# Kernel optimization log

Measured on AMD Instinct MI355X. Metric: run time of the kernel, lower is better.

The kernel has to match this reference:

```python
import jax, jax.numpy as jnp
import numpy as np

B, T, E, H = 4, 2048, 1024, 1024

def setup_inputs() -> dict:
    key = jax.random.key(0)
    k1, k2, k3, k4 = jax.random.split(key, 4)
    inputs = jax.random.normal(k1, (B, T, E), dtype=jnp.float32)
    # Dense(size, use_bias=False) -> weight [emb, size], glorot-ish scale
    Wq = jax.random.normal(k2, (E, H), dtype=jnp.float32) * (1.0 / np.sqrt(E))
    Wk = jax.random.normal(k3, (E, H), dtype=jnp.float32) * (1.0 / np.sqrt(E))
    Wv = jax.random.normal(k4, (E, H), dtype=jnp.float32) * (1.0 / np.sqrt(E))
    return {"inputs": inputs, "Wq": Wq, "Wk": Wk, "Wv": Wv}

def reference(inputs, Wq, Wk, Wv):
    # inputs: [B, T, E]
    _, Tc, Ec = inputs.shape
    q = inputs @ Wq  # [B, T, H]
    k = inputs @ Wk  # [B, T, H]
    v = inputs @ Wv  # [B, T, H]
    # scores scaled by emb_dim**-0.5 (NOT head size) as in the source
    w = jnp.einsum('bih,bjh->bij', q, k) * (Ec ** -0.5)  # [B, T, T]
    tril = jnp.tril(jnp.ones((Tc, Tc), dtype=bool))
    w = jnp.where(tril, w, -jnp.inf)
    # NOTE: source uses softmax over axis=1 (query axis), non-standard but faithful
    w = jax.nn.softmax(w, axis=1)
    # dropout_rate=0.0 -> identity
    out = w @ v  # [B, T, H]
    return out
```

## Files before the change

### kernel.cpp

```cpp
#include <hip/hip_runtime.h>
#include <hip/hip_bf16.h>
#include <stdint.h>


typedef short bf16x8 __attribute__((ext_vector_type(8)));
typedef float f32x4  __attribute__((ext_vector_type(4)));

__device__ __forceinline__ unsigned short f2bf(float f) {
    union { float f; unsigned u; } x; x.f = f;
    unsigned r = x.u + 0x7FFFu + ((x.u >> 16) & 1u);
    return (unsigned short)(r >> 16);
}
__device__ __forceinline__ float bf2f(unsigned short h) {
    union { unsigned u; float f; } x; x.u = ((unsigned)h) << 16;
    return x.f;
}

__global__ __launch_bounds__(256) void prep_kernel(
    const float* __restrict__ X,
    const float* __restrict__ Wq, const float* __restrict__ Wk,
    const float* __restrict__ Wv,
    unsigned short* __restrict__ Xb, unsigned short* __restrict__ WT)
{
    __shared__ unsigned short tile[64][65];
    unsigned id = blockIdx.x;
    if (id < 8192) {
        size_t i = ((size_t)id * 256 + threadIdx.x) * 4;
        float4 v = *(const float4*)(X + i);
        union { unsigned short h[4]; unsigned long long u; } p;
        p.h[0] = f2bf(v.x); p.h[1] = f2bf(v.y);
        p.h[2] = f2bf(v.z); p.h[3] = f2bf(v.w);
        *(unsigned long long*)(Xb + i) = p.u;
    } else {
        unsigned w = id - 8192;
        unsigned which = w >> 8;
        const float* W = (which == 0) ? Wq : (which == 1) ? Wk : Wv;
        unsigned short* out = WT + (size_t)which * 1024 * 1024;
        const int R = 1024, C = 1024;
        unsigned t2 = w & 255;
        int c0 = (int)(t2 & 15) * 64, r0 = (int)(t2 >> 4) * 64;
        int tx = threadIdx.x & 63, ty = threadIdx.x >> 6;
#pragma unroll
        for (int i = 0; i < 16; ++i) {
            int r = ty + i * 4;
            tile[r][tx] = f2bf(W[(size_t)(r0 + r) * C + c0 + tx]);
        }
        __syncthreads();
#pragma unroll
        for (int i = 0; i < 16; ++i) {
            int c = ty + i * 4;
            out[(size_t)(c0 + c) * R + r0 + tx] = tile[tx][c];
        }
    }
}

__global__ __launch_bounds__(256, 3) void gemm_nt_qkv(
    const unsigned short* __restrict__ A, const unsigned short* __restrict__ B,
    unsigned short* __restrict__ Cout, unsigned short* __restrict__ C2,
    unsigned short* __restrict__ C3, int K, int ldt)
{
    unsigned id = blockIdx.y * gridDim.x + blockIdx.x;
    unsigned xcd = id & 7, k2 = id >> 3;
    int tm = (int)(xcd * 8 + (k2 & 7));
    int tn = (int)(k2 >> 3);
    int m0 = tm * 128, n0 = tn * 128;
    int kmax = K;

    __shared__ unsigned short sAB[2 * 128 * 64];
    char* sAc = (char*)sAB;
    char* sBc = (char*)sAB + 16384;

    unsigned t = threadIdx.x, lane = t & 63, wave = t >> 6;

    unsigned srow = t >> 2;
    unsigned gsw = (t & 3) ^ ((t >> 3) & 3);
    const unsigned short* pA = A + (size_t)(m0 + srow) * K + gsw * 8;
    const unsigned short* pB = B + (size_t)(n0 + srow) * K + gsw * 8;
    const size_t rstep = (size_t)64 * K;
    unsigned ldsOff = t * 16;

    unsigned wm = (wave >> 1) * 64, wn = (wave & 1) * 64;
    unsigned lrow = lane & 15;
    unsigned lk = ((lane >> 4) ^ ((lane >> 1) & 3)) * 8;
    const short* sAs = (const short*)sAB;
    const short* sBs = (const short*)(sAB + 128 * 64);

    f32x4 acc[4][4] = {};

    int4 rA0 = *(const int4*)(pA);
    int4 rA1 = *(const int4*)(pA + rstep);
    int4 rA2 = *(const int4*)(pA + 32);
    int4 rA3 = *(const int4*)(pA + rstep + 32);
    int4 rB0 = *(const int4*)(pB);
    int4 rB1 = *(const int4*)(pB + rstep);
    int4 rB2 = *(const int4*)(pB + 32);
    int4 rB3 = *(const int4*)(pB + rstep + 32);

    for (int k0 = 0; k0 < kmax; k0 += 64) {
        __syncthreads();
        *(int4*)(sAc + ldsOff)         = rA0;
        *(int4*)(sAc + ldsOff + 4096)  = rA1;
        *(int4*)(sAc + ldsOff + 8192)  = rA2;
        *(int4*)(sAc + ldsOff + 12288) = rA3;
        *(int4*)(sBc + ldsOff)         = rB0;
        *(int4*)(sBc + ldsOff + 4096)  = rB1;
        *(int4*)(sBc + ldsOff + 8192)  = rB2;
        *(int4*)(sBc + ldsOff + 12288) = rB3;
        __syncthreads();

        if (k0 + 64 < kmax) {
            pA += 64; pB += 64;
            rA0 = *(const int4*)(pA);
            rA1 = *(const int4*)(pA + rstep);
            rA2 = *(const int4*)(pA + 32);
            rA3 = *(const int4*)(pA + rstep + 32);
            rB0 = *(const int4*)(pB);
            rB1 = *(const int4*)(pB + rstep);
            rB2 = *(const int4*)(pB + 32);
            rB3 = *(const int4*)(pB + rstep + 32);
        }

#pragma unroll
        for (int kk = 0; kk < 2; ++kk) {
            bf16x8 a[4], b[4];
#pragma unroll
            for (int i = 0; i < 4; ++i) {
                a[i] = *(const bf16x8*)(sAs + kk * 4096 + (wm + i * 16 + lrow) * 32 + lk);
                b[i] = *(const bf16x8*)(sBs + kk * 4096 + (wn + i * 16 + lrow) * 32 + lk);
            }
#pragma unroll
            for (int i = 0; i < 4; ++i)
#pragma unroll
                for (int j = 0; j < 4; ++j)
                    acc[i][j] = __builtin_amdgcn_mfma_f32_16x16x32_bf16(
                        a[i], b[j], acc[i][j], 0, 0, 0);
        }
    }

    unsigned col = lane & 15, rq = (lane >> 4) * 4;
    if (n0 < 2048) {
        unsigned short* C = (n0 < 1024) ? Cout : C2;
        int nb = n0 & 1023;
#pragma unroll
        for (int i = 0; i < 4; ++i)
#pragma unroll
            for (int j = 0; j < 4; ++j)
#pragma unroll
                for (int r = 0; r < 4; ++r)
                    C[(size_t)(m0 + wm + i * 16 + rq + r) * 1024 + nb + wn + j * 16 + col] =
                        f2bf(acc[i][j][r]);
    } else {
        int batch = m0 >> 11, tb = m0 & 2047;
        unsigned short* C = C3 + (size_t)batch * 1024 * 2048;
#pragma unroll
        for (int i = 0; i < 4; ++i)
#pragma unroll
            for (int j = 0; j < 4; ++j) {
                union { unsigned short h[4]; unsigned long long u; } p;
#pragma unroll
                for (int r = 0; r < 4; ++r) p.h[r] = f2bf(acc[i][j][r]);
                int h = (n0 - 2048) + wn + j * 16 + col;
                int t0 = tb + wm + i * 16 + rq;
                *(unsigned long long*)(C + (size_t)h * ldt + t0) = p.u;
            }
    }
}

__global__ __launch_bounds__(256, 4) void scores64_kernel(
    const unsigned short* __restrict__ A, const unsigned short* __restrict__ B,
    unsigned short* __restrict__ Eb, float* __restrict__ fpar, float scale)
{
    int bz = blockIdx.z;
    unsigned bx = blockIdx.x;
    int u = (int)((bx & 7u) * 34u + (bx >> 3));
    int tm = (int)((sqrtf(4.f * (float)u + 1.f) - 1.f) * 0.5f);
    while ((tm + 1) * (tm + 2) <= u) ++tm;
    while (tm * (tm + 1) > u) --tm;
    int tn64 = u - tm * (tm + 1);
    const int K = 1024;
    int m0 = tm * 128, n0 = tn64 * 64;
    A += (size_t)bz * (size_t)2048 * 1024;
    B += (size_t)bz * (size_t)2048 * 1024;

    __shared__ unsigned short sAB[12288];
    char* sAc = (char*)sAB;
    char* sBc = (char*)sAB + 16384;

    unsigned t = threadIdx.x, lane = t & 63, wave = t >> 6;
    unsigned srow = t >> 2;
    unsigned gsw = (t & 3) ^ ((t >> 3) & 3);
    const unsigned short* pA = A + (size_t)(m0 + srow) * K + gsw * 8;
    const unsigned short* pB = B + (size_t)(n0 + srow) * K + gsw * 8;
    const size_t rstep = (size_t)64 * K;
    unsigned ldsOff = t * 16;

    unsigned wm = (wave >> 1) * 64, wn = (wave & 1) * 32;
    unsigned lrow = lane & 15;
    unsigned lk = ((lane >> 4) ^ ((lane >> 1) & 3)) * 8;
    const short* sAs = (const short*)sAB;
    const short* sBs = (const short*)(sAB + 8192);

    f32x4 acc[4][2] = {};

    int4 rA0 = *(const int4*)(pA);
    int4 rA1 = *(const int4*)(pA + rstep);
    int4 rA2 = *(const int4*)(pA + 32);
    int4 rA3 = *(const int4*)(pA + rstep + 32);
    int4 rB0 = *(const int4*)(pB);
    int4 rB1 = *(const int4*)(pB + 32);

    for (int k0 = 0; k0 < K; k0 += 64) {
        __syncthreads();
        *(int4*)(sAc + ldsOff)         = rA0;
        *(int4*)(sAc + ldsOff + 4096)  = rA1;
        *(int4*)(sAc + ldsOff + 8192)  = rA2;
        *(int4*)(sAc + ldsOff + 12288) = rA3;
        *(int4*)(sBc + ldsOff)         = rB0;
        *(int4*)(sBc + ldsOff + 4096)  = rB1;
        __syncthreads();

        if (k0 + 64 < K) {
            pA += 64; pB += 64;
            rA0 = *(const int4*)(pA);
            rA1 = *(const int4*)(pA + rstep);
            rA2 = *(const int4*)(pA + 32);
            rA3 = *(const int4*)(pA + rstep + 32);
            rB0 = *(const int4*)(pB);
            rB1 = *(const int4*)(pB + 32);
        }

#pragma unroll
        for (int kk = 0; kk < 2; ++kk) {
            bf16x8 a[4], b[2];
#pragma unroll
            for (int i = 0; i < 4; ++i)
                a[i] = *(const bf16x8*)(sAs + kk * 4096 + (wm + i * 16 + lrow) * 32 + lk);
#pragma unroll
            for (int j = 0; j < 2; ++j)
                b[j] = *(const bf16x8*)(sBs + kk * 2048 + (wn + j * 16 + lrow) * 32 + lk);
#pragma unroll
            for (int i = 0; i < 4; ++i)
#pragma unroll
                for (int j = 0; j < 2; ++j)
                    acc[i][j] = __builtin_amdgcn_mfma_f32_16x16x32_bf16(
                        a[i], b[j], acc[i][j], 0, 0, 0);
        }
    }

    unsigned col = lane & 15, rq = (lane >> 4) * 4;
    unsigned short* Ebp = Eb + (size_t)bz * (size_t)2048 * 2048;
    float* par = fpar + (size_t)bz * 32 * 2048;
    bool diag = ((tn64 >> 1) == tm);
    unsigned short* tile = sAB;
    __syncthreads();
#pragma unroll
    for (int jj = 0; jj < 2; ++jj) {
        float csum = 0.f;
        int jl = (int)(wn + jj * 16 + col);
        int jg = n0 + jl;
#pragma unroll
        for (int ii = 0; ii < 4; ++ii) {
#pragma unroll
            for (int r = 0; r < 4; ++r) {
                int il = (int)(wm + ii * 16 + rq + r);
                int ig = m0 + il;
                unsigned short us = 0;
                if (!diag || ig >= jg)
                    us = f2bf(__expf(acc[ii][jj][r] * scale));
                tile[il * 64 + jl] = us;
                csum += bf2f(us);
            }
        }
        csum += __shfl_xor(csum, 16);
        csum += __shfl_xor(csum, 32);
        if (lane < 16) {
            int rh = (m0 + (int)wm) >> 6;
            par[(size_t)rh * 2048 + n0 + wn + jj * 16 + lane] = csum;
        }
    }
    __syncthreads();
    {
        unsigned rr = t >> 3, cc = (t & 7) * 8;
#pragma unroll
        for (int p = 0; p < 4; ++p) {
            int li = (int)(p * 32 + rr);
            int4 v = *(const int4*)(tile + li * 64 + cc);
            *(int4*)(Ebp + (size_t)(m0 + li) * 2048 + n0 + cc) = v;
        }
    }
}

__global__ __launch_bounds__(256, 4) void pv64_kernel(
    const unsigned short* __restrict__ A, const unsigned short* __restrict__ B,
    float* __restrict__ out)
{
    unsigned id = blockIdx.x;
    int tm = 15 - (int)(id >> 6);
    unsigned rest = id & 63u;
    int bz = (int)(rest >> 4);
    int tn64 = (int)(rest & 15u);
    const int K = 2048;
    int m0 = tm * 128, n0 = tn64 * 64;
    int kmax = m0 + 128;
    A += (size_t)bz * (size_t)2048 * 2048;
    B += (size_t)bz * (size_t)1024 * 2048;

    __shared__ unsigned short sAB[12288];
    char* sAc = (char*)sAB;
    char* sBc = (char*)sAB + 16384;

    unsigned t = threadIdx.x, lane = t & 63, wave = t >> 6;
    unsigned srow = t >> 2;
    unsigned gsw = (t & 3) ^ ((t >> 3) & 3);
    const unsigned short* pA = A + (size_t)(m0 + srow) * K + gsw * 8;
    const unsigned short* pB = B + (size_t)(n0 + srow) * K + gsw * 8;
    const size_t rstep = (size_t)64 * K;
    unsigned ldsOff = t * 16;

    unsigned wm = (wave >> 1) * 64, wn = (wave & 1) * 32;
    unsigned lrow = lane & 15;
    unsigned lk = ((lane >> 4) ^ ((lane >> 1) & 3)) * 8;
    const short* sAs = (const short*)sAB;
    const short* sBs = (const short*)(sAB + 8192);

    f32x4 acc[4][2] = {};

    int4 rA0 = *(const int4*)(pA);
    int4 rA1 = *(const int4*)(pA + rstep);
    int4 rA2 = *(const int4*)(pA + 32);
    int4 rA3 = *(const int4*)(pA + rstep + 32);
    int4 rB0 = *(const int4*)(pB);
    int4 rB1 = *(const int4*)(pB + 32);

    for (int k0 = 0; k0 < kmax; k0 += 64) {
        __syncthreads();
        *(int4*)(sAc + ldsOff)         = rA0;
        *(int4*)(sAc + ldsOff + 4096)  = rA1;
        *(int4*)(sAc + ldsOff + 8192)  = rA2;
        *(int4*)(sAc + ldsOff + 12288) = rA3;
        *(int4*)(sBc + ldsOff)         = rB0;
        *(int4*)(sBc + ldsOff + 4096)  = rB1;
        __syncthreads();

        if (k0 + 64 < kmax) {
            pA += 64; pB += 64;
            rA0 = *(const int4*)(pA);
            rA1 = *(const int4*)(pA + rstep);
            rA2 = *(const int4*)(pA + 32);
            rA3 = *(const int4*)(pA + rstep + 32);
            rB0 = *(const int4*)(pB);
            rB1 = *(const int4*)(pB + 32);
        }

#pragma unroll
        for (int kk = 0; kk < 2; ++kk) {
            bf16x8 a[4], b[2];
#pragma unroll
            for (int i = 0; i < 4; ++i)
                a[i] = *(const bf16x8*)(sAs + kk * 4096 + (wm + i * 16 + lrow) * 32 + lk);
#pragma unroll
            for (int j = 0; j < 2; ++j)
                b[j] = *(const bf16x8*)(sBs + kk * 2048 + (wn + j * 16 + lrow) * 32 + lk);
#pragma unroll
            for (int i = 0; i < 4; ++i)
#pragma unroll
                for (int j = 0; j < 2; ++j)
                    acc[i][j] = __builtin_amdgcn_mfma_f32_16x16x32_bf16(
                        a[i], b[j], acc[i][j], 0, 0, 0);
        }
    }

    unsigned col = lane & 15, rq = (lane >> 4) * 4;
    float* C = out + (size_t)bz * (size_t)2048 * 1024;
#pragma unroll
    for (int i = 0; i < 4; ++i)
#pragma unroll
        for (int j = 0; j < 2; ++j)
#pragma unroll
            for (int r = 0; r < 4; ++r)
                C[(size_t)(m0 + wm + i * 16 + rq + r) * 1024 + n0 + wn + j * 16 + col] =
                    acc[i][j][r];
}

__global__ __launch_bounds__(256) void colsum_scale(
    const float* __restrict__ par, unsigned short* __restrict__ Vt)
{
    int b = blockIdx.z, t0 = blockIdx.x * 64, h0 = blockIdx.y * 128;
    __shared__ float Ls[64];
    int tid = threadIdx.x;
    if (tid < 64) {
        int j = t0 + tid;
        const float* p = par + (size_t)b * 32 * 2048;
        float s = 0.f;
        for (int rh = j >> 6; rh < 32; ++rh) s += p[(size_t)rh * 2048 + j];
        Ls[tid] = 1.0f / s;
    }
    __syncthreads();
    unsigned short* V = Vt + ((size_t)b << 21);
    int c8 = (tid & 7) * 8;
#pragma unroll
    for (int rr = 0; rr < 4; ++rr) {
        int h = h0 + rr * 32 + (tid >> 3);
        size_t idx = (size_t)h * 2048 + t0 + c8;
        bf16x8 v = *(bf16x8*)(V + idx);
#pragma unroll
        for (int e = 0; e < 8; ++e)
            v[e] = (short)f2bf(bf2f((unsigned short)v[e]) * Ls[c8 + e]);
        *(bf16x8*)(V + idx) = v;
    }
}

extern "C" void kernel_launch(void* const* d_in, const int* in_sizes, int n_in,
                              void* d_out, int out_size, void* d_ws, size_t ws_size,
                              hipStream_t stream)
{
    const int B = 4, T = 2048, E = 1024, H = 1024;
    const int M = B * T;
    const float* X  = (const float*)d_in[0];
    const float* Wq = (const float*)d_in[1];
    const float* Wk = (const float*)d_in[2];
    const float* Wv = (const float*)d_in[3];
    float* out = (float*)d_out;
    char* ws = (char*)d_ws;
    const size_t MB = 1024 * 1024;

    unsigned short* Xb  = (unsigned short*)(ws + 0);
    unsigned short* WqT = (unsigned short*)(ws + 16 * MB);
    unsigned short* Qb  = (unsigned short*)(ws + 32 * MB);
    unsigned short* Kb  = (unsigned short*)(ws + 48 * MB);
    unsigned short* Vt  = (unsigned short*)(ws + 64 * MB);
    unsigned short* Eb  = (unsigned short*)(ws + 0);
    float*          par  = (float*)d_out;

    prep_kernel<<<dim3(8960), 256, 0, stream>>>(X, Wq, Wk, Wv, Xb, WqT);

    gemm_nt_qkv<<<dim3(24, 64, 1), 256, 0, stream>>>(
        Xb, WqT, Qb, Kb, Vt, E, T);

    scores64_kernel<<<dim3(272, 1, B), 256, 0, stream>>>(
        Qb, Kb, Eb, par, 0.03125f);

    colsum_scale<<<dim3(32, 8, 4), 256, 0, stream>>>(par, Vt);

    pv64_kernel<<<dim3(1024), 256, 0, stream>>>(Eb, Vt, out);
}
```

Measured before the change: 233.6 us.

## Widen PV GEMM tile to 128x128 and split QKV GEMM into two launches

The causal P·V kernel now uses 128x128 output tiles with a 4x4 MFMA accumulator per wave, replacing the 128x64 tiles. This halves the block count and doubles reuse of each loaded A tile. The blocks are ordered so that long and short causal rows from different batches pair up. Separately, the QKV projection GEMM is split into two launches over halves of the M tiles. This costs an extra launch and lowers occupancy in the PV kernel, since each thread holds more registers.

```diff
diff --git a/kernel.cpp b/kernel.cpp
--- a/kernel.cpp
+++ b/kernel.cpp
@@ -57,12 +57,12 @@
 __global__ __launch_bounds__(256, 3) void gemm_nt_qkv(
     const unsigned short* __restrict__ A, const unsigned short* __restrict__ B,
     unsigned short* __restrict__ Cout, unsigned short* __restrict__ C2,
-    unsigned short* __restrict__ C3, int K, int ldt)
+    unsigned short* __restrict__ C3, int K, int ldt, int tmoff)
 {
     unsigned id = blockIdx.y * gridDim.x + blockIdx.x;
     unsigned xcd = id & 7, k2 = id >> 3;
-    int tm = (int)(xcd * 8 + (k2 & 7));
-    int tn = (int)(k2 >> 3);
+    int tm = (int)(xcd * 4 + (k2 & 3)) + tmoff;
+    int tn = (int)(k2 >> 2);
     int m0 = tm * 128, n0 = tn * 128;
     int kmax = K;
 
@@ -290,26 +290,27 @@
     }
 }
 
-__global__ __launch_bounds__(256, 4) void pv64_kernel(
+__global__ __launch_bounds__(256, 3) void pv128_kernel(
     const unsigned short* __restrict__ A, const unsigned short* __restrict__ B,
     float* __restrict__ out)
 {
-    unsigned id = blockIdx.x;
-    int tm = 15 - (int)(id >> 6);
-    unsigned rest = id & 63u;
-    int bz = (int)(rest >> 4);
-    int tn64 = (int)(rest & 15u);
-    const int K = 2048;
-    int m0 = tm * 128, n0 = tn64 * 64;
+    unsigned n = blockIdx.x;
+    int tn = (int)(n & 7u);
+    unsigned q = n >> 3, half = q >> 5, r = q & 31u;
+    int bz = (int)((half ? 2u : 0u) + (r & 1u));
+    int tm = half ? (int)(r >> 1) : (int)(15u - (r >> 1));
+    const int K = 2048, N = 1024;
+    int m0 = tm * 128, n0 = tn * 128;
     int kmax = m0 + 128;
     A += (size_t)bz * (size_t)2048 * 2048;
     B += (size_t)bz * (size_t)1024 * 2048;
 
-    __shared__ unsigned short sAB[12288];
+    __shared__ unsigned short sAB[2 * 128 * 64];
     char* sAc = (char*)sAB;
     char* sBc = (char*)sAB + 16384;
 
     unsigned t = threadIdx.x, lane = t & 63, wave = t >> 6;
+
     unsigned srow = t >> 2;
     unsigned gsw = (t & 3) ^ ((t >> 3) & 3);
     const unsigned short* pA = A + (size_t)(m0 + srow) * K + gsw * 8;
@@ -317,20 +318,22 @@
     const size_t rstep = (size_t)64 * K;
     unsigned ldsOff = t * 16;
 
-    unsigned wm = (wave >> 1) * 64, wn = (wave & 1) * 32;
+    unsigned wm = (wave >> 1) * 64, wn = (wave & 1) * 64;
     unsigned lrow = lane & 15;
     unsigned lk = ((lane >> 4) ^ ((lane >> 1) & 3)) * 8;
     const short* sAs = (const short*)sAB;
-    const short* sBs = (const short*)(sAB + 8192);
-
-    f32x4 acc[4][2] = {};
+    const short* sBs = (const short*)(sAB + 128 * 64);
+
+    f32x4 acc[4][4] = {};
 
     int4 rA0 = *(const int4*)(pA);
     int4 rA1 = *(const int4*)(pA + rstep);
     int4 rA2 = *(const int4*)(pA + 32);
     int4 rA3 = *(const int4*)(pA + rstep + 32);
     int4 rB0 = *(const int4*)(pB);
-    int4 rB1 = *(const int4*)(pB + 32);
+    int4 rB1 = *(const int4*)(pB + rstep);
+    int4 rB2 = *(const int4*)(pB + 32);
+    int4 rB3 = *(const int4*)(pB + rstep + 32);
 
     for (int k0 = 0; k0 < kmax; k0 += 64) {
         __syncthreads();
@@ -340,6 +343,8 @@
         *(int4*)(sAc + ldsOff + 12288) = rA3;
         *(int4*)(sBc + ldsOff)         = rB0;
         *(int4*)(sBc + ldsOff + 4096)  = rB1;
+        *(int4*)(sBc + ldsOff + 8192)  = rB2;
+        *(int4*)(sBc + ldsOff + 12288) = rB3;
         __syncthreads();
 
         if (k0 + 64 < kmax) {
@@ -349,22 +354,23 @@
             rA2 = *(const int4*)(pA + 32);
             rA3 = *(const int4*)(pA + rstep + 32);
             rB0 = *(const int4*)(pB);
-            rB1 = *(const int4*)(pB + 32);
+            rB1 = *(const int4*)(pB + rstep);
+            rB2 = *(const int4*)(pB + 32);
+            rB3 = *(const int4*)(pB + rstep + 32);
         }
 
 #pragma unroll
         for (int kk = 0; kk < 2; ++kk) {
-            bf16x8 a[4], b[2];
+            bf16x8 a[4], b[4];
+#pragma unroll
+            for (int i = 0; i < 4; ++i) {
+                a[i] = *(const bf16x8*)(sAs + kk * 4096 + (wm + i * 16 + lrow) * 32 + lk);
+                b[i] = *(const bf16x8*)(sBs + kk * 4096 + (wn + i * 16 + lrow) * 32 + lk);
+            }
 #pragma unroll
             for (int i = 0; i < 4; ++i)
-                a[i] = *(const bf16x8*)(sAs + kk * 4096 + (wm + i * 16 + lrow) * 32 + lk);
-#pragma unroll
-            for (int j = 0; j < 2; ++j)
-                b[j] = *(const bf16x8*)(sBs + kk * 2048 + (wn + j * 16 + lrow) * 32 + lk);
-#pragma unroll
-            for (int i = 0; i < 4; ++i)
-#pragma unroll
-                for (int j = 0; j < 2; ++j)
+#pragma unroll
+                for (int j = 0; j < 4; ++j)
                     acc[i][j] = __builtin_amdgcn_mfma_f32_16x16x32_bf16(
                         a[i], b[j], acc[i][j], 0, 0, 0);
         }
@@ -375,10 +381,10 @@
 #pragma unroll
     for (int i = 0; i < 4; ++i)
 #pragma unroll
-        for (int j = 0; j < 2; ++j)
+        for (int j = 0; j < 4; ++j)
 #pragma unroll
             for (int r = 0; r < 4; ++r)
-                C[(size_t)(m0 + wm + i * 16 + rq + r) * 1024 + n0 + wn + j * 16 + col] =
+                C[(size_t)(m0 + wm + i * 16 + rq + r) * N + n0 + wn + j * 16 + col] =
                     acc[i][j][r];
 }
 
@@ -434,13 +440,15 @@
 
     prep_kernel<<<dim3(8960), 256, 0, stream>>>(X, Wq, Wk, Wv, Xb, WqT);
 
-    gemm_nt_qkv<<<dim3(24, 64, 1), 256, 0, stream>>>(
-        Xb, WqT, Qb, Kb, Vt, E, T);
+    gemm_nt_qkv<<<dim3(24, 32, 1), 256, 0, stream>>>(
+        Xb, WqT, Qb, Kb, Vt, E, T, 0);
+    gemm_nt_qkv<<<dim3(24, 32, 1), 256, 0, stream>>>(
+        Xb, WqT, Qb, Kb, Vt, E, T, 32);
 
     scores64_kernel<<<dim3(272, 1, B), 256, 0, stream>>>(
         Qb, Kb, Eb, par, 0.03125f);
 
     colsum_scale<<<dim3(32, 8, 4), 256, 0, stream>>>(par, Vt);
 
-    pv64_kernel<<<dim3(1024), 256, 0, stream>>>(Eb, Vt, out);
-}
+    pv128_kernel<<<dim3(512), 256, 0, stream>>>(Eb, Vt, out);
+}
```

Result: no change. 235.3 us (+0.7%).
